# Kernel tuning notes

Measured on AMD Instinct MI355X. Metric: run time of the kernel, lower is better.

## Reference

```python
import jax, jax.numpy as jnp
import numpy as np

IN_DIMS = (32, 64, 96, 128)
N_EXPERTS = len(IN_DIMS)
MAX_F = max(IN_DIMS)
D = 2 * MAX_F
N = 8192
TOP_K = 2
H_DIM = 1024
OUT_DIM = 768
LN_EPS = 1e-6


def _build_mask():
    # mask[f] = [1]*s + [0]*(MAX_F-s) + [1]*s + [0]*(MAX_F-s), shape (E, 1, D)
    m = np.zeros((N_EXPERTS, 1, D), dtype=np.float32)
    for i, s in enumerate(IN_DIMS):
        m[i, 0, :s] = 1.0
        m[i, 0, MAX_F:MAX_F + s] = 1.0
    return jnp.asarray(m)

_MASK = _build_mask()


def _multi_in_expert(x_final, expert_weights, expert_indices, W, b):
    """MoE dispatch/combine of MultiInSizeLinear (expert_indices path).
    x_final: (E, N, D); expert_weights/indices: (N, K); W: (E, O, D); b: (E, O)."""
    Wm = W * _MASK                                   # (E, O, D) masked per-size weights
    # per-expert outputs for every token (the torch loop computes these per mask group)
    Y = jnp.einsum('end,eod->eno', x_final, Wm) + b[:, None, :]   # (E, N, O)
    valid = expert_indices < N_EXPERTS               # (N, K) real-expert mask
    rsum = jnp.sum(expert_weights * valid, axis=-1, keepdims=True)
    rsum = jnp.where(rsum == 0, 1.0, rsum)
    wnorm = jnp.where(valid, expert_weights / rsum, 0.0)          # (N, K)
    safe = jnp.where(valid, expert_indices, 0)
    n_idx = jnp.arange(Y.shape[1])
    gathered = Y[safe, n_idx[:, None]]               # (N, K, O)
    return jnp.sum(wnorm[..., None] * gathered, axis=1)           # (N, O)


def setup_inputs() -> dict:
    key = jax.random.key(0)
    ks = jax.random.split(key, 12)
    s_hid = 1.0 / np.sqrt(D)
    s_out = 1.0 / np.sqrt(H_DIM)
    return {
        'x': jax.random.normal(ks[0], (N, D), jnp.float32),
        'in_feat_size': jax.random.randint(ks[1], (N,), 0, MAX_F, jnp.int64) if jax.config.jax_enable_x64 else jax.random.randint(ks[1], (N,), 0, MAX_F, jnp.int32),
        'expert_weights': jax.random.uniform(ks[2], (N, TOP_K), jnp.float32),
        'expert_indices': jax.random.randint(ks[3], (N, TOP_K), 0, 6, jnp.int32),
        'x_final': jax.random.normal(ks[4], (N_EXPERTS, N, D), jnp.float32),
        'W_hid': jax.random.normal(ks[5], (N_EXPERTS, H_DIM, D), jnp.float32) * s_hid,
        'b_hid': jax.random.normal(ks[6], (N_EXPERTS, H_DIM), jnp.float32) * s_hid,
        'W_out': jax.random.normal(ks[7], (OUT_DIM, H_DIM), jnp.float32) * s_out,
        'b_out': jax.random.normal(ks[8], (OUT_DIM,), jnp.float32) * s_out,
        'W_res': jax.random.normal(ks[9], (N_EXPERTS, OUT_DIM, D), jnp.float32) * s_hid,
        'b_res': jax.random.normal(ks[10], (N_EXPERTS, OUT_DIM), jnp.float32) * s_hid,
        'ln_w': jnp.ones((OUT_DIM,), jnp.float32),
    }


def reference(x, in_feat_size, expert_weights, expert_indices, x_final,
              W_hid, b_hid, W_out, b_out, W_res, b_res, ln_w):
    xf = jnp.nan_to_num(x_final, nan=0.0)
    hid = _multi_in_expert(xf, expert_weights, expert_indices, W_hid, b_hid)
    hid = jax.nn.gelu(hid, approximate=False)
    out = hid @ W_out.T + b_out                      # output_layer (dropout p=0 -> identity)
    res = _multi_in_expert(xf, expert_weights, expert_indices, W_res, b_res)
    out = out + res
    # T5LayerNorm (RMSNorm)
    var = jnp.mean(out * out, axis=-1, keepdims=True)
    return ln_w * (out * jax.lax.rsqrt(var + LN_EPS))
```

## Files before the change

### kernel.cpp

```cpp
#include <hip/hip_runtime.h>
#include <hip/hip_bf16.h>

#define TOKENS 8192
#define D_IN   256
#define HDIM   1024
#define ODIM   768
#define KPACK  704
#define NCHUNK 88

typedef short bf16x8 __attribute__((ext_vector_type(8)));
typedef float f32x4  __attribute__((ext_vector_type(4)));

static __device__ __forceinline__ ushort f2b(float f) {
    union { __hip_bfloat16 b; ushort u; } cv;
    cv.b = __float2bfloat16(f);
    return cv.u;
}
static __device__ __forceinline__ float b2f(ushort u) {
    union { ushort u; __hip_bfloat16 b; } cv;
    cv.u = u;
    return __bfloat162float(cv.b);
}

static __device__ __forceinline__ void chunk_map(int c8, int& e, int& d0) {
    int cc;
    if (c8 < 8)       { e = 0; cc = c8; }
    else if (c8 < 24) { e = 1; cc = c8 - 8; }
    else if (c8 < 48) { e = 2; cc = c8 - 24; }
    else              { e = 3; cc = c8 - 48; }
    int half = 4 * (e + 1);
    d0 = (cc < half) ? cc * 8 : 128 + (cc - half) * 8;
}

static __device__ __forceinline__ void stage16(const ushort* g, ushort* l) {
    __builtin_amdgcn_global_load_lds(
        (const __attribute__((address_space(1))) void*)g,
        (__attribute__((address_space(3))) void*)l, 16, 0, 0);
}

static __device__ __forceinline__ float gelu_f(float v) {
    float y = 0.7978845608f * v * (1.f + 0.044715f * v * v);
    return v - v / (__expf(2.f * y) + 1.f);
}

__global__ __launch_bounds__(256) void k_pack_a(
    const float* __restrict__ ew, const int* __restrict__ ei,
    const float* __restrict__ xf, ushort* __restrict__ Ap) {
    int gid = blockIdx.x * 256 + threadIdx.x;
    int n  = gid / NCHUNK;
    int c8 = gid - n * NCHUNK;
    int   i0 = ei[2 * n], i1 = ei[2 * n + 1];
    float w0 = ew[2 * n], w1 = ew[2 * n + 1];
    bool v0 = (unsigned)i0 < 4u, v1 = (unsigned)i1 < 4u;
    float rs = (v0 ? w0 : 0.f) + (v1 ? w1 : 0.f);
    if (rs == 0.f) rs = 1.f;
    float o0 = v0 ? w0 / rs : 0.f;
    float o1 = v1 ? w1 / rs : 0.f;
    ushort o[8] __attribute__((aligned(16))) = {0, 0, 0, 0, 0, 0, 0, 0};
    if (c8 < 80) {
        int e, d0;
        chunk_map(c8, e, d0);
        float w = ((v0 && i0 == e) ? o0 : 0.f) + ((v1 && i1 == e) ? o1 : 0.f);
        if (w != 0.f) {
            const float* s = xf + ((size_t)e * TOKENS + n) * D_IN + d0;
#pragma unroll
            for (int j = 0; j < 8; ++j) {
                float v = s[j];
                if (!(v == v)) v = 0.f;
                o[j] = f2b(w * v);
            }
        }
    } else if (c8 == 80) {
#pragma unroll
        for (int j = 0; j < 4; ++j) {
            float m = ((v0 && i0 == j) ? o0 : 0.f) + ((v1 && i1 == j) ? o1 : 0.f);
            o[j] = f2b(m);
        }
    }
    *(uint4*)(Ap + (size_t)n * KPACK + c8 * 8) = *(const uint4*)o;
}

#define BW_SPLIT (1792 * NCHUNK)
__global__ __launch_bounds__(256) void k_pack_bw(
    const float* __restrict__ Whid, const float* __restrict__ bhid,
    const float* __restrict__ Wres, const float* __restrict__ bres,
    const float* __restrict__ Wout,
    ushort* __restrict__ Bp, ushort* __restrict__ Wb) {
    int gid = blockIdx.x * 256 + threadIdx.x;
    if (gid < BW_SPLIT) {
        int o_ = gid / NCHUNK;
        int c8 = gid - o_ * NCHUNK;
        ushort v[8] __attribute__((aligned(16))) = {0, 0, 0, 0, 0, 0, 0, 0};
        if (c8 < 80) {
            int e, d0;
            chunk_map(c8, e, d0);
            const float* s = (o_ < HDIM)
                ? Whid + ((size_t)e * HDIM + o_) * D_IN + d0
                : Wres + ((size_t)e * ODIM + (o_ - HDIM)) * D_IN + d0;
#pragma unroll
            for (int j = 0; j < 8; ++j) v[j] = f2b(s[j]);
        } else if (c8 == 80) {
#pragma unroll
            for (int j = 0; j < 4; ++j) {
                float b = (o_ < HDIM) ? bhid[j * HDIM + o_] : bres[j * ODIM + (o_ - HDIM)];
                v[j] = f2b(b);
            }
        }
        *(uint4*)(Bp + (size_t)o_ * KPACK + c8 * 8) = *(const uint4*)v;
    } else {
        int g2 = gid - BW_SPLIT;
        const float* s = Wout + (size_t)g2 * 8;
        ushort v[8] __attribute__((aligned(16)));
#pragma unroll
        for (int j = 0; j < 8; ++j) v[j] = f2b(s[j]);
        *(uint4*)(Wb + (size_t)g2 * 8) = *(const uint4*)v;
    }
}

__global__ __launch_bounds__(512, 2) void k_gemm1(
    const ushort* __restrict__ A, const ushort* __restrict__ B,
    ushort* __restrict__ hidB, ushort* __restrict__ resb) {
    __shared__ __align__(16) ushort As[2][256 * 64];
    __shared__ __align__(16) ushort Bs[2][256 * 64];
    const int tid = threadIdx.x;
    const int lane = tid & 63, w = tid >> 6;
    const int wr = w >> 2, wc = w & 3;
    const int r = lane & 15, g = lane >> 4;
    const int sx = r & 7;

    int bid  = blockIdx.x;
    int widx = (bid & 7) * 28 + (bid >> 3);
    int bm = widx / 7, bn = widx - bm * 7;

    const int srow = tid >> 3;
    const int gc   = (tid & 7) ^ (srow & 7);
    const int wv8  = w * 8;
    const ushort* Abase = A + (size_t)(bm * 256) * KPACK;
    const ushort* Bbase = B + (size_t)(bn * 256) * KPACK;

#define STG(gsrc, grow, kc, lds, lrow)                                      \
    stage16((gsrc) + (size_t)((grow) + srow) * KPACK + ((kc) + gc) * 8,     \
            (lds) + ((lrow) + wv8) * 64)

    STG(Bbase, 0, 0, &Bs[0][0], 0);     STG(Bbase, 64, 0, &Bs[0][0], 64);
    STG(Bbase, 128, 0, &Bs[0][0], 128); STG(Bbase, 192, 0, &Bs[0][0], 192);
    STG(Abase, 0, 0, &As[0][0], 0);     STG(Abase, 64, 0, &As[0][0], 64);
    STG(Abase, 128, 0, &As[0][0], 128); STG(Abase, 192, 0, &As[0][0], 192);
    STG(Bbase, 0, 8, &Bs[1][0], 0);     STG(Bbase, 64, 8, &Bs[1][0], 64);
    STG(Bbase, 128, 8, &Bs[1][0], 128); STG(Bbase, 192, 8, &Bs[1][0], 192);
    STG(Abase, 0, 8, &As[1][0], 0);     STG(Abase, 128, 8, &As[1][0], 128);
    asm volatile("s_waitcnt vmcnt(6)" ::: "memory");
    __builtin_amdgcn_s_barrier();

    f32x4 acc[8][4] = {};
    bf16x8 af[2][2], bfr[4][2];

#define LD_A(buf, mi, ks) (*(const bf16x8*)&As[buf][(wr * 128 + (mi) * 16 + r) * 64 + ((((ks) * 4 + g) ^ sx) * 8)])
#define LD_B(buf, j, ks)  (*(const bf16x8*)&Bs[buf][(wc * 64  + (j) * 16 + r) * 64 + ((((ks) * 4 + g) ^ sx) * 8)])
#define READ_A(buf, qq) do {                                                  \
    af[0][0] = LD_A(buf, 2 * (qq), 0);     af[0][1] = LD_A(buf, 2 * (qq), 1); \
    af[1][0] = LD_A(buf, 2 * (qq) + 1, 0); af[1][1] = LD_A(buf, 2 * (qq) + 1, 1); } while (0)
#define READ_B(buf) do { _Pragma("unroll")                                   \
    for (int j_ = 0; j_ < 4; ++j_) { bfr[j_][0] = LD_B(buf, j_, 0); bfr[j_][1] = LD_B(buf, j_, 1); } } while (0)
#define MFMA_Q(qq) do {                                                      \
    __builtin_amdgcn_s_setprio(1);                                           \
    _Pragma("unroll") for (int i_ = 0; i_ < 2; ++i_)                         \
    _Pragma("unroll") for (int k_ = 0; k_ < 2; ++k_)                         \
    _Pragma("unroll") for (int j_ = 0; j_ < 4; ++j_)                         \
        acc[2 * (qq) + i_][j_] = __builtin_amdgcn_mfma_f32_16x16x32_bf16(    \
            af[i_][k_], bfr[j_][k_], acc[2 * (qq) + i_][j_], 0, 0, 0);       \
    __builtin_amdgcn_s_setprio(0); } while (0)
#define OPEN_BAR() do { __builtin_amdgcn_sched_barrier(0);                   \
    __builtin_amdgcn_s_barrier(); } while (0)

#pragma unroll
    for (int i = 0; i < 5; ++i) {
        const int kcp = (2 * i + 1) * 8;
        const int kc0 = (2 * i + 2) * 8;
        const int kc1 = (2 * i + 3) * 8;
        const bool st1 = (i < 4);
        READ_B(0); READ_A(0, 0);
        STG(Abase, 64, kcp, &As[1][0], 64);
        STG(Abase, 192, kcp, &As[1][0], 192);
        OPEN_BAR(); MFMA_Q(0); __builtin_amdgcn_s_barrier();
        READ_A(0, 1);
        STG(Bbase, 0, kc0, &Bs[0][0], 0);
        STG(Bbase, 64, kc0, &Bs[0][0], 64);
        OPEN_BAR(); MFMA_Q(1);
        READ_A(0, 2);
        STG(Bbase, 128, kc0, &Bs[0][0], 128);
        STG(Bbase, 192, kc0, &Bs[0][0], 192);
        OPEN_BAR(); MFMA_Q(2);
        READ_A(0, 3);
        STG(Abase, 0, kc0, &As[0][0], 0);
        STG(Abase, 128, kc0, &As[0][0], 128);
        OPEN_BAR(); MFMA_Q(3);
        asm volatile("s_waitcnt vmcnt(6)" ::: "memory");
        __builtin_amdgcn_s_barrier();
        READ_B(1); READ_A(1, 0);
        STG(Abase, 64, kc0, &As[0][0], 64);
        STG(Abase, 192, kc0, &As[0][0], 192);
        OPEN_BAR(); MFMA_Q(0); __builtin_amdgcn_s_barrier();
        READ_A(1, 1);
        if (st1) { STG(Bbase, 0, kc1, &Bs[1][0], 0);
                   STG(Bbase, 64, kc1, &Bs[1][0], 64); }
        OPEN_BAR(); MFMA_Q(1);
        READ_A(1, 2);
        if (st1) { STG(Bbase, 128, kc1, &Bs[1][0], 128);
                   STG(Bbase, 192, kc1, &Bs[1][0], 192); }
        OPEN_BAR(); MFMA_Q(2);
        READ_A(1, 3);
        if (st1) { STG(Abase, 0, kc1, &As[1][0], 0);
                   STG(Abase, 128, kc1, &As[1][0], 128); }
        OPEN_BAR(); MFMA_Q(3);
        if (st1) asm volatile("s_waitcnt vmcnt(6)" ::: "memory");
        else     asm volatile("s_waitcnt vmcnt(0)" ::: "memory");
        __builtin_amdgcn_s_barrier();
    }
    READ_B(0); READ_A(0, 0); MFMA_Q(0);
    READ_A(0, 1); MFMA_Q(1);
    READ_A(0, 2); MFMA_Q(2);
    READ_A(0, 3); MFMA_Q(3);
#undef STG
#undef LD_A
#undef LD_B
#undef READ_A
#undef READ_B
#undef MFMA_Q
#undef OPEN_BAR

#pragma unroll
    for (int fi = 0; fi < 8; ++fi) {
#pragma unroll
        for (int j = 0; j < 4; ++j) {
            int col = bn * 256 + wc * 64 + j * 16 + r;
#pragma unroll
            for (int qq = 0; qq < 4; ++qq) {
                int row = bm * 256 + wr * 128 + fi * 16 + g * 4 + qq;
                float v = acc[fi][j][qq];
                if (col < HDIM) {
                    hidB[(size_t)row * HDIM + col] = f2b(gelu_f(v));
                } else {
                    resb[(size_t)row * ODIM + (col - HDIM)] = f2b(v);
                }
            }
        }
    }
}

__global__ __launch_bounds__(256, 2) void k_gemm2(
    const ushort* __restrict__ A, const ushort* __restrict__ B,
    const float* __restrict__ bout, const ushort* __restrict__ resb,
    ushort* __restrict__ outb) {
    __shared__ __align__(16) ushort As[2][128 * 64];
    __shared__ __align__(16) ushort Bs[2][128 * 64];
    const int tid = threadIdx.x;
    const int lane = tid & 63, w = tid >> 6;
    const int wr = w >> 1, wc = w & 1;
    const int r = lane & 15, g = lane >> 4;
    const int bm = blockIdx.x, bn = blockIdx.y;

    const int srow = tid >> 3;
    const int gc   = (tid & 7) ^ (srow & 7);
    const ushort* Ag = A + (size_t)(bm * 128 + srow) * HDIM + gc * 8;
    const ushort* Bg = B + (size_t)(bn * 128 + srow) * HDIM + gc * 8;
    const int ldst = (w * 8) * 64;

#define G2_STAGE(p, kt) do {                                            \
    _Pragma("unroll")                                                   \
    for (int i_ = 0; i_ < 4; ++i_) {                                    \
        stage16(Ag + (size_t)(i_ * 32) * HDIM + (kt), &As[p][ldst + i_ * 32 * 64]); \
        stage16(Bg + (size_t)(i_ * 32) * HDIM + (kt), &Bs[p][ldst + i_ * 32 * 64]); \
    } } while (0)

    G2_STAGE(0, 0);
    G2_STAGE(1, 64);

    f32x4 acc[4][4] = {};
    const int cA = (wr * 64 + r) * 64;
    const int cB = (wc * 64 + r) * 64;
    const int sx = r & 7;
    const int cs0 = ((0 * 4 + g) ^ sx) * 8;
    const int cs1 = ((1 * 4 + g) ^ sx) * 8;

    int cur = 0;
#pragma unroll
    for (int t = 0; t < 16; ++t) {
        if (t < 15) asm volatile("s_waitcnt vmcnt(8)" ::: "memory");
        else        asm volatile("s_waitcnt vmcnt(0)" ::: "memory");
        __builtin_amdgcn_s_barrier();
        const ushort* Ab = As[cur];
        const ushort* Bb = Bs[cur];
        bf16x8 a0[4], b0[4], a1[4], b1[4];
#pragma unroll
        for (int j = 0; j < 4; ++j) {
            b0[j] = *(const bf16x8*)&Bb[cB + j * 16 * 64 + cs0];
            b1[j] = *(const bf16x8*)&Bb[cB + j * 16 * 64 + cs1];
        }
#pragma unroll
        for (int i = 0; i < 4; ++i) {
            a0[i] = *(const bf16x8*)&Ab[cA + i * 16 * 64 + cs0];
            a1[i] = *(const bf16x8*)&Ab[cA + i * 16 * 64 + cs1];
        }
        asm volatile("s_waitcnt lgkmcnt(0)" ::: "memory");
        __builtin_amdgcn_sched_barrier(0);
        __builtin_amdgcn_s_barrier();
        if (t + 2 < 16) G2_STAGE(cur, (t + 2) * 64);
        __builtin_amdgcn_s_setprio(1);
#pragma unroll
        for (int i = 0; i < 4; ++i)
#pragma unroll
            for (int j = 0; j < 4; ++j)
                acc[i][j] = __builtin_amdgcn_mfma_f32_16x16x32_bf16(
                    a0[i], b0[j], acc[i][j], 0, 0, 0);
#pragma unroll
        for (int i = 0; i < 4; ++i)
#pragma unroll
            for (int j = 0; j < 4; ++j)
                acc[i][j] = __builtin_amdgcn_mfma_f32_16x16x32_bf16(
                    a1[i], b1[j], acc[i][j], 0, 0, 0);
        __builtin_amdgcn_s_setprio(0);
        cur ^= 1;
    }
#undef G2_STAGE

#pragma unroll
    for (int fi = 0; fi < 4; ++fi) {
#pragma unroll
        for (int j = 0; j < 4; ++j) {
            int col = bn * 128 + wc * 64 + j * 16 + r;
#pragma unroll
            for (int qq = 0; qq < 4; ++qq) {
                int row = bm * 128 + wr * 64 + fi * 16 + g * 4 + qq;
                size_t idx = (size_t)row * ODIM + col;
                float v = acc[fi][j][qq] + bout[col] + b2f(resb[idx]);
                outb[idx] = f2b(v);
            }
        }
    }
}

__global__ __launch_bounds__(256) void k_rms(
    const ushort* __restrict__ outb, const float* __restrict__ lnw,
    float* __restrict__ out) {
    int row = blockIdx.x, t = threadIdx.x;
    const ushort* p = outb + (size_t)row * ODIM;
    float v0 = b2f(p[t]), v1 = b2f(p[t + 256]), v2 = b2f(p[t + 512]);
    float s = v0 * v0 + v1 * v1 + v2 * v2;
#pragma unroll
    for (int off = 32; off > 0; off >>= 1) s += __shfl_down(s, off, 64);
    __shared__ float ws4[4];
    if ((t & 63) == 0) ws4[t >> 6] = s;
    __syncthreads();
    float tot = ws4[0] + ws4[1] + ws4[2] + ws4[3];
    float sc = rsqrtf(tot * (1.f / 768.f) + 1e-6f);
    out[(size_t)row * ODIM + t]       = lnw[t]       * v0 * sc;
    out[(size_t)row * ODIM + t + 256] = lnw[t + 256] * v1 * sc;
    out[(size_t)row * ODIM + t + 512] = lnw[t + 512] * v2 * sc;
}

extern "C" void kernel_launch(void* const* d_in, const int* in_sizes, int n_in,
                              void* d_out, int out_size, void* d_ws, size_t ws_size,
                              hipStream_t stream) {
    const float* ew   = (const float*)d_in[2];
    const int*   ei   = (const int*)d_in[3];
    const float* xf   = (const float*)d_in[4];
    const float* Whid = (const float*)d_in[5];
    const float* bhid = (const float*)d_in[6];
    const float* Wout = (const float*)d_in[7];
    const float* bout = (const float*)d_in[8];
    const float* Wres = (const float*)d_in[9];
    const float* bres = (const float*)d_in[10];
    const float* lnw  = (const float*)d_in[11];

    char* ws = (char*)d_ws;
    ushort* Ap   = (ushort*)(ws);
    ushort* Bp   = (ushort*)(ws + 11534336);
    ushort* Wb   = (ushort*)(ws + 14057472);
    ushort* hidB = (ushort*)(ws + 15630336);
    ushort* resb = (ushort*)(ws + 32407552);
    ushort* outb = (ushort*)(ws + 44990464);

    k_pack_a<<<2816, 256, 0, stream>>>(ew, ei, xf, Ap);
    k_pack_bw<<<1000, 256, 0, stream>>>(Whid, bhid, Wres, bres, Wout, Bp, Wb);
    k_gemm1<<<224, 512, 0, stream>>>(Ap, Bp, hidB, resb);
    k_gemm2<<<dim3(64, 6), 256, 0, stream>>>(hidB, Wb, bout, resb, outb);
    k_rms<<<8192, 256, 0, stream>>>(outb, lnw, (float*)d_out);
}
```

Baseline: 74.06 us.

## Replace fine-grained interleaved staging with simple double-buffered K-loop

Replaces the hand-interleaved schedule, in which global-to-LDS stages were spread between MFMA quarters with many barriers, with a plain double-buffered loop over 11 K-chunks. Each iteration reads LDS and runs all MFMAs, then barriers, issues the next-but-one chunk's loads into the freed buffer, and waits until the next buffer is ready. This cuts the barrier count and simplifies the schedule, but each stage now issues at a single point instead of being spread across compute, which risks exposing more load latency.

```diff
diff --git a/kernel.cpp b/kernel.cpp
--- a/kernel.cpp
+++ b/kernel.cpp
@@ -141,19 +141,18 @@
 #define STG(gsrc, grow, kc, lds, lrow)                                      \
     stage16((gsrc) + (size_t)((grow) + srow) * KPACK + ((kc) + gc) * 8,     \
             (lds) + ((lrow) + wv8) * 64)
-
-    STG(Bbase, 0, 0, &Bs[0][0], 0);     STG(Bbase, 64, 0, &Bs[0][0], 64);
-    STG(Bbase, 128, 0, &Bs[0][0], 128); STG(Bbase, 192, 0, &Bs[0][0], 192);
-    STG(Abase, 0, 0, &As[0][0], 0);     STG(Abase, 64, 0, &As[0][0], 64);
-    STG(Abase, 128, 0, &As[0][0], 128); STG(Abase, 192, 0, &As[0][0], 192);
-    STG(Bbase, 0, 8, &Bs[1][0], 0);     STG(Bbase, 64, 8, &Bs[1][0], 64);
-    STG(Bbase, 128, 8, &Bs[1][0], 128); STG(Bbase, 192, 8, &Bs[1][0], 192);
-    STG(Abase, 0, 8, &As[1][0], 0);     STG(Abase, 128, 8, &As[1][0], 128);
-    asm volatile("s_waitcnt vmcnt(6)" ::: "memory");
+#define STG8(p, kc) do {                                                    \
+    STG(Abase, 0, kc, &As[p][0], 0);     STG(Abase, 64, kc, &As[p][0], 64); \
+    STG(Abase, 128, kc, &As[p][0], 128); STG(Abase, 192, kc, &As[p][0], 192);\
+    STG(Bbase, 0, kc, &Bs[p][0], 0);     STG(Bbase, 64, kc, &Bs[p][0], 64); \
+    STG(Bbase, 128, kc, &Bs[p][0], 128); STG(Bbase, 192, kc, &Bs[p][0], 192);} while (0)
+
+    STG8(0, 0);
+    STG8(1, 8);
+    asm volatile("s_waitcnt vmcnt(8)" ::: "memory");
     __builtin_amdgcn_s_barrier();
 
     f32x4 acc[8][4] = {};
-    bf16x8 af[2][2], bfr[4][2];
 
 #define LD_A(buf, mi, ks) (*(const bf16x8*)&As[buf][(wr * 128 + (mi) * 16 + r) * 64 + ((((ks) * 4 + g) ^ sx) * 8)])
 #define LD_B(buf, j, ks)  (*(const bf16x8*)&Bs[buf][(wc * 64  + (j) * 16 + r) * 64 + ((((ks) * 4 + g) ^ sx) * 8)])
@@ -163,71 +162,44 @@
 #define READ_B(buf) do { _Pragma("unroll")                                   \
     for (int j_ = 0; j_ < 4; ++j_) { bfr[j_][0] = LD_B(buf, j_, 0); bfr[j_][1] = LD_B(buf, j_, 1); } } while (0)
 #define MFMA_Q(qq) do {                                                      \
-    __builtin_amdgcn_s_setprio(1);                                           \
     _Pragma("unroll") for (int i_ = 0; i_ < 2; ++i_)                         \
     _Pragma("unroll") for (int k_ = 0; k_ < 2; ++k_)                         \
     _Pragma("unroll") for (int j_ = 0; j_ < 4; ++j_)                         \
         acc[2 * (qq) + i_][j_] = __builtin_amdgcn_mfma_f32_16x16x32_bf16(    \
             af[i_][k_], bfr[j_][k_], acc[2 * (qq) + i_][j_], 0, 0, 0);       \
-    __builtin_amdgcn_s_setprio(0); } while (0)
-#define OPEN_BAR() do { __builtin_amdgcn_sched_barrier(0);                   \
-    __builtin_amdgcn_s_barrier(); } while (0)
-
-#pragma unroll
-    for (int i = 0; i < 5; ++i) {
-        const int kcp = (2 * i + 1) * 8;
-        const int kc0 = (2 * i + 2) * 8;
-        const int kc1 = (2 * i + 3) * 8;
-        const bool st1 = (i < 4);
-        READ_B(0); READ_A(0, 0);
-        STG(Abase, 64, kcp, &As[1][0], 64);
-        STG(Abase, 192, kcp, &As[1][0], 192);
-        OPEN_BAR(); MFMA_Q(0); __builtin_amdgcn_s_barrier();
-        READ_A(0, 1);
-        STG(Bbase, 0, kc0, &Bs[0][0], 0);
-        STG(Bbase, 64, kc0, &Bs[0][0], 64);
-        OPEN_BAR(); MFMA_Q(1);
-        READ_A(0, 2);
-        STG(Bbase, 128, kc0, &Bs[0][0], 128);
-        STG(Bbase, 192, kc0, &Bs[0][0], 192);
-        OPEN_BAR(); MFMA_Q(2);
-        READ_A(0, 3);
-        STG(Abase, 0, kc0, &As[0][0], 0);
-        STG(Abase, 128, kc0, &As[0][0], 128);
-        OPEN_BAR(); MFMA_Q(3);
-        asm volatile("s_waitcnt vmcnt(6)" ::: "memory");
-        __builtin_amdgcn_s_barrier();
-        READ_B(1); READ_A(1, 0);
-        STG(Abase, 64, kc0, &As[0][0], 64);
-        STG(Abase, 192, kc0, &As[0][0], 192);
-        OPEN_BAR(); MFMA_Q(0); __builtin_amdgcn_s_barrier();
-        READ_A(1, 1);
-        if (st1) { STG(Bbase, 0, kc1, &Bs[1][0], 0);
-                   STG(Bbase, 64, kc1, &Bs[1][0], 64); }
-        OPEN_BAR(); MFMA_Q(1);
-        READ_A(1, 2);
-        if (st1) { STG(Bbase, 128, kc1, &Bs[1][0], 128);
-                   STG(Bbase, 192, kc1, &Bs[1][0], 192); }
-        OPEN_BAR(); MFMA_Q(2);
-        READ_A(1, 3);
-        if (st1) { STG(Abase, 0, kc1, &As[1][0], 0);
-                   STG(Abase, 128, kc1, &As[1][0], 128); }
-        OPEN_BAR(); MFMA_Q(3);
-        if (st1) asm volatile("s_waitcnt vmcnt(6)" ::: "memory");
-        else     asm volatile("s_waitcnt vmcnt(0)" ::: "memory");
-        __builtin_amdgcn_s_barrier();
-    }
-    READ_B(0); READ_A(0, 0); MFMA_Q(0);
-    READ_A(0, 1); MFMA_Q(1);
-    READ_A(0, 2); MFMA_Q(2);
-    READ_A(0, 3); MFMA_Q(3);
+    } while (0)
+
+#pragma unroll
+    for (int t = 0; t < 11; ++t) {
+        const int buf = t & 1;
+        bf16x8 af[2][2], bfr[4][2];
+        __builtin_amdgcn_s_setprio(1);
+        READ_B(buf);
+        READ_A(buf, 0); MFMA_Q(0);
+        READ_A(buf, 1); MFMA_Q(1);
+        READ_A(buf, 2); MFMA_Q(2);
+        READ_A(buf, 3); MFMA_Q(3);
+        __builtin_amdgcn_s_setprio(0);
+        if (t < 10) {
+            asm volatile("s_waitcnt lgkmcnt(0)" ::: "memory");
+            __builtin_amdgcn_sched_barrier(0);
+            __builtin_amdgcn_s_barrier();
+            if (t + 2 <= 10) {
+                STG8(buf, (t + 2) * 8);
+                asm volatile("s_waitcnt vmcnt(8)" ::: "memory");
+            } else {
+                asm volatile("s_waitcnt vmcnt(0)" ::: "memory");
+            }
+            __builtin_amdgcn_s_barrier();
+        }
+    }
 #undef STG
+#undef STG8
 #undef LD_A
 #undef LD_B
 #undef READ_A
 #undef READ_B
 #undef MFMA_Q
-#undef OPEN_BAR
 
 #pragma unroll
     for (int fi = 0; fi < 8; ++fi) {
```

New measurement: 77.16 us. 1.04x slower.
